# Optimization experiments

Measured on AMD Instinct MI355X. Metric: run time of the kernel, lower is better.

The kernel has to match this reference:

```python
import jax, jax.numpy as jnp
import numpy as np

B, N, C, DFF, NH, KNN = 4, 2048, 256, 1024, 4, 16


def _gelu(x):
    return jax.nn.gelu(x, approximate=False)  # torch nn.GELU default = exact erf


def _ln(x, g, b, eps=1e-5):
    m = jnp.mean(x, axis=-1, keepdims=True)
    v = jnp.mean((x - m) ** 2, axis=-1, keepdims=True)
    return (x - m) * jax.lax.rsqrt(v + eps) * g + b


def setup_inputs() -> dict:
    key = jax.random.key(0)
    ks = jax.random.split(key, 16)
    w = lambda k, shp: jax.random.normal(k, shp, jnp.float32) * 0.02
    return {
        "src1": jax.random.normal(ks[0], (B, C, N), jnp.float32),
        "src2": jax.random.normal(ks[1], (B, C, N), jnp.float32),
        "pos": jax.random.uniform(ks[2], (B, 3, N), jnp.float32),
        # input_proj Conv1d(C, C, 1)
        "Wp": w(ks[3], (C, C)), "bp": jnp.zeros((C,), jnp.float32),
        # rel_pos_encoder: Conv2d(3, C//4, 1) -> GELU -> Conv2d(C//4, 1, 1)
        "Wr1": w(ks[4], (C // 4, 3)), "br1": jnp.zeros((C // 4,), jnp.float32),
        "Wr2": w(ks[5], (1, C // 4)), "br2": jnp.zeros((1,), jnp.float32),
        # MultiheadAttention packed in-proj + out-proj
        "Wqkv": w(ks[6], (3 * C, C)), "bqkv": jnp.zeros((3 * C,), jnp.float32),
        "Wo": w(ks[7], (C, C)), "bo": jnp.zeros((C,), jnp.float32),
        # norms
        "g13": jnp.ones((C,), jnp.float32), "b13": jnp.zeros((C,), jnp.float32),
        "g12": jnp.ones((C,), jnp.float32), "b12": jnp.zeros((C,), jnp.float32),
        # FFN
        "W1": w(ks[8], (DFF, C)), "b1": jnp.zeros((DFF,), jnp.float32),
        "W2": w(ks[9], (C, DFF)), "b2": jnp.zeros((C,), jnp.float32),
    }


def reference(src1, src2, pos, Wp, bp, Wr1, br1, Wr2, br2, Wqkv, bqkv,
              Wo, bo, g13, b13, g12, b12, W1, b1, W2, b2):
    b, _, n = src1.shape
    c = Wp.shape[0]
    h = NH
    dh = c // h

    # input_proj (1x1 conv == matmul over channel dim); go to (b, n, c)
    s1 = jnp.einsum('oc,bcn->bno', Wp, src1) + bp
    s2 = jnp.einsum('oc,bcn->bno', Wp, src2) + bp

    # --- KNN + rel-pos bias ---
    p = pos.transpose(0, 2, 1)  # (b, n, 3)
    sq = jnp.sum(p * p, axis=-1)  # (b, n)
    dist = sq[:, :, None] + sq[:, None, :] - 2.0 * jnp.einsum('bnd,bmd->bnm', p, p)
    _, idx = jax.lax.top_k(-dist, KNN)  # (b, n, KNN) nearest (incl. self)
    knn_pos = jax.vmap(lambda pp, ii: pp[ii])(p, idx)  # (b, n, KNN, 3)
    rel = p[:, :, None, :] - knn_pos  # (b, n, KNN, 3)
    hid = _gelu(jnp.einsum('bnkd,od->bnko', rel, Wr1) + br1)
    bias_vals = (jnp.einsum('bnko,uo->bnku', hid, Wr2) + br2)[..., 0]  # (b, n, KNN)

    attn_bias = jnp.full((b, n, n), -jnp.inf, dtype=s1.dtype)
    bi = jnp.arange(b)[:, None, None]
    ri = jnp.arange(n)[None, :, None]
    attn_bias = attn_bias.at[bi, ri, idx].set(bias_vals)  # scatter along dim 2

    # --- pre-norm (norm13 shared for q and kv) ---
    x1 = _ln(s1, g13, b13)
    x2 = _ln(s2, g13, b13)

    # --- multihead attention with additive float mask ---
    Wq, Wk, Wv = jnp.split(Wqkv, 3, axis=0)
    bq, bk, bv = jnp.split(bqkv, 3)
    q = (x1 @ Wq.T + bq).reshape(b, n, h, dh)
    k = (x2 @ Wk.T + bk).reshape(b, n, h, dh)
    v = (x2 @ Wv.T + bv).reshape(b, n, h, dh)
    scores = jnp.einsum('bqhd,bkhd->bhqk', q, k) / jnp.sqrt(jnp.asarray(dh, s1.dtype))
    scores = scores + attn_bias[:, None, :, :]  # repeat_interleave(nhead) == head broadcast
    attn = jax.nn.softmax(scores, axis=-1)
    o = jnp.einsum('bhqk,bkhd->bqhd', attn, v).reshape(b, n, c) @ Wo.T + bo

    x1 = _ln(x1 + o, g12, b12)
    ff = _gelu(x1 @ W1.T + b1) @ W2.T + b2
    out = x1 + ff
    return out.transpose(0, 2, 1)  # (b, c, n)
```

## Files before the change

kernel.cpp:

```cpp
#include <hip/hip_runtime.h>
#include <hip/hip_bf16.h>
#include <math.h>

constexpr int kB = 4;
constexpr int kN = 2048;
constexpr int kC = 256;
constexpr int kDFF = 1024;
constexpr int kKNN = 16;
constexpr int kDH = 64;

typedef __attribute__((ext_vector_type(8))) short short8;
typedef __attribute__((ext_vector_type(4))) float float4v;

__device__ __forceinline__ float gelu_erf(float x) {
    return 0.5f * x * (1.0f + erff(x * 0.70710678118654752440f));
}

__device__ __forceinline__ short f2b(float f) {
    unsigned u = __float_as_uint(f);
    u = u + 0x7FFFu + ((u >> 16) & 1u);
    return (short)(u >> 16);
}

__device__ __forceinline__ float b2f(short h) {
    unsigned u = ((unsigned)(unsigned short)h) << 16;
    return __uint_as_float(u);
}

__global__ __launch_bounds__(256) void cvt_all(
    const float* __restrict__ Wqkv, const float* __restrict__ Wo,
    const float* __restrict__ W1, const float* __restrict__ W2,
    const float* __restrict__ Wp, short* __restrict__ dst)
{
    const int i = (blockIdx.x * 256 + threadIdx.x) * 8;
    if (i < 786432) {
        const float* src; int off;
        if (i < 196608)      { src = Wqkv; off = i; }
        else if (i < 262144) { src = Wo;   off = i - 196608; }
        else if (i < 524288) { src = W1;   off = i - 262144; }
        else                 { src = W2;   off = i - 524288; }
        short8 v;
        #pragma unroll
        for (int j = 0; j < 8; j++) v[j] = f2b(src[off + j]);
        *(short8*)&dst[i] = v;
    } else {
        const int off = i - 786432;
        short8 h, l;
        #pragma unroll
        for (int j = 0; j < 8; j++) {
            float v = Wp[off + j];
            short hh = f2b(v);
            h[j] = hh;
            l[j] = f2b(v - b2f(hh));
        }
        *(short8*)&dst[786432 + off] = h;
        *(short8*)&dst[851968 + off] = l;
    }
}

__global__ __launch_bounds__(256) void transpose_cvt(
    const float* __restrict__ src1, const float* __restrict__ src2,
    short* __restrict__ hiT, short* __restrict__ loT)
{
    __shared__ float tile[32][33];
    const int z = blockIdx.z;
    const float* in = (z < 4 ? src1 : src2) + (size_t)(z & 3) * kC * kN;
    const int n0 = blockIdx.x * 32;
    const int c0 = blockIdx.y * 32;
    const int tx = threadIdx.x;
    const int ty = threadIdx.y;
    #pragma unroll
    for (int i = 0; i < 32; i += 8)
        tile[ty + i][tx] = in[(size_t)(c0 + ty + i) * kN + (n0 + tx)];
    __syncthreads();
    #pragma unroll
    for (int i = 0; i < 32; i += 8) {
        float v = tile[tx][ty + i];
        short h = f2b(v);
        short l = f2b(v - b2f(h));
        size_t o = ((size_t)z * kN + (n0 + ty + i)) * kC + (c0 + tx);
        hiT[o] = h;
        loT[o] = l;
    }
}

__global__ __launch_bounds__(256) void proj_mfma(
    const short* __restrict__ Ahi, const short* __restrict__ Alo,
    const short* __restrict__ Whi, const short* __restrict__ Wlo,
    const float* __restrict__ bias, float* __restrict__ out)
{
    __shared__ __align__(16) short AsmH[64][40], AsmL[64][40];
    __shared__ __align__(16) short BsmH[64][40], BsmL[64][40];

    const int tid = threadIdx.x;
    const int n0 = blockIdx.x * 64;
    const size_t m0 = (size_t)blockIdx.y * 64;
    const int lane = tid & 63, wv = tid >> 6;
    const int lm = lane & 15, quad = lane >> 4;
    const int r = tid >> 2, q = tid & 3;

    float4v acc[4] = {};

    for (int k0 = 0; k0 < kC; k0 += 32) {
        *(short8*)&AsmH[r][q * 8] = *(const short8*)&Ahi[(m0 + r) * kC + k0 + q * 8];
        *(short8*)&AsmL[r][q * 8] = *(const short8*)&Alo[(m0 + r) * kC + k0 + q * 8];
        *(short8*)&BsmH[r][q * 8] = *(const short8*)&Whi[(size_t)(n0 + r) * kC + k0 + q * 8];
        *(short8*)&BsmL[r][q * 8] = *(const short8*)&Wlo[(size_t)(n0 + r) * kC + k0 + q * 8];
        __syncthreads();

        short8 ah = *(const short8*)&AsmH[wv * 16 + lm][quad * 8];
        short8 al = *(const short8*)&AsmL[wv * 16 + lm][quad * 8];
        #pragma unroll
        for (int j4 = 0; j4 < 4; j4++) {
            short8 bh = *(const short8*)&BsmH[j4 * 16 + lm][quad * 8];
            short8 bl = *(const short8*)&BsmL[j4 * 16 + lm][quad * 8];
            acc[j4] = __builtin_amdgcn_mfma_f32_16x16x32_bf16(al, bh, acc[j4], 0, 0, 0);
            acc[j4] = __builtin_amdgcn_mfma_f32_16x16x32_bf16(ah, bl, acc[j4], 0, 0, 0);
            acc[j4] = __builtin_amdgcn_mfma_f32_16x16x32_bf16(ah, bh, acc[j4], 0, 0, 0);
        }
        __syncthreads();
    }

    #pragma unroll
    for (int j4 = 0; j4 < 4; j4++) {
        const int n = n0 + j4 * 16 + lm;
        const float bn = bias[n];
        #pragma unroll
        for (int rg = 0; rg < 4; rg++) {
            const size_t m = m0 + wv * 16 + quad * 4 + rg;
            out[m * kC + n] = acc[j4][rg] + bn;
        }
    }
}

__global__ __launch_bounds__(256) void mfma_gemm_bf(
    const short* __restrict__ A, const short* __restrict__ W,
    const float* __restrict__ bias, const float* __restrict__ resid,
    float* __restrict__ out, short* __restrict__ outbf,
    int M, int Nout, int K, int epi)
{
    __shared__ __align__(16) short Asm[64][40];
    __shared__ __align__(16) short Bsm[64][40];

    const int tid = threadIdx.x;
    const int n0 = blockIdx.x * 64;
    const int m0 = blockIdx.y * 64;
    const int lane = tid & 63, wv = tid >> 6;
    const int lm = lane & 15, quad = lane >> 4;
    const int r = tid >> 2, q = tid & 3;

    float4v acc[4] = {};

    for (int k0 = 0; k0 < K; k0 += 32) {
        *(short8*)&Asm[r][q * 8] = *(const short8*)&A[(size_t)(m0 + r) * K + k0 + q * 8];
        *(short8*)&Bsm[r][q * 8] = *(const short8*)&W[(size_t)(n0 + r) * K + k0 + q * 8];
        __syncthreads();

        short8 af = *(const short8*)&Asm[wv * 16 + lm][quad * 8];
        #pragma unroll
        for (int j4 = 0; j4 < 4; j4++) {
            short8 bf = *(const short8*)&Bsm[j4 * 16 + lm][quad * 8];
            acc[j4] = __builtin_amdgcn_mfma_f32_16x16x32_bf16(af, bf, acc[j4], 0, 0, 0);
        }
        __syncthreads();
    }

    #pragma unroll
    for (int j4 = 0; j4 < 4; j4++) {
        const int n = n0 + j4 * 16 + lm;
        const float bn = bias[n];
        #pragma unroll
        for (int rg = 0; rg < 4; rg++) {
            const int m = m0 + wv * 16 + quad * 4 + rg;
            float v = acc[j4][rg] + bn;
            if (resid) v += resid[(size_t)m * Nout + n];
            if (epi == 1) v = gelu_erf(v);
            if (out)   out[(size_t)m * Nout + n] = v;
            if (outbf) outbf[(size_t)m * Nout + n] = f2b(v);
        }
    }
}

__global__ __launch_bounds__(256) void qkv_gemm(
    const short* __restrict__ x1bf, const short* __restrict__ x2bf,
    const short* __restrict__ Wqkvbf, const float* __restrict__ bqkv,
    float* __restrict__ qb, float* __restrict__ kvb)
{
    __shared__ __align__(16) short Asm[64][40];
    __shared__ __align__(16) short Bsm[64][40];

    const int n0g = blockIdx.x * 64;
    const int m0 = blockIdx.y * 64;
    const short* A; float* out; int Nout; int ncol0;
    if (n0g < 256) { A = x1bf; out = qb;  Nout = 256; ncol0 = n0g; }
    else           { A = x2bf; out = kvb; Nout = 512; ncol0 = n0g - 256; }

    const int tid = threadIdx.x;
    const int lane = tid & 63, wv = tid >> 6;
    const int lm = lane & 15, quad = lane >> 4;
    const int r = tid >> 2, q = tid & 3;

    float4v acc[4] = {};

    for (int k0 = 0; k0 < kC; k0 += 32) {
        *(short8*)&Asm[r][q * 8] = *(const short8*)&A[(size_t)(m0 + r) * kC + k0 + q * 8];
        *(short8*)&Bsm[r][q * 8] = *(const short8*)&Wqkvbf[(size_t)(n0g + r) * kC + k0 + q * 8];
        __syncthreads();

        short8 af = *(const short8*)&Asm[wv * 16 + lm][quad * 8];
        #pragma unroll
        for (int j4 = 0; j4 < 4; j4++) {
            short8 bf = *(const short8*)&Bsm[j4 * 16 + lm][quad * 8];
            acc[j4] = __builtin_amdgcn_mfma_f32_16x16x32_bf16(af, bf, acc[j4], 0, 0, 0);
        }
        __syncthreads();
    }

    #pragma unroll
    for (int j4 = 0; j4 < 4; j4++) {
        const int nc = ncol0 + j4 * 16 + lm;
        const float bn = bqkv[n0g + j4 * 16 + lm];
        #pragma unroll
        for (int rg = 0; rg < 4; rg++) {
            const int m = m0 + wv * 16 + quad * 4 + rg;
            out[(size_t)m * Nout + nc] = acc[j4][rg] + bn;
        }
    }
}

__global__ __launch_bounds__(256) void ln_kernel(
    float* __restrict__ x, short* __restrict__ xbf,
    const float* __restrict__ g, const float* __restrict__ bb)
{
    const size_t row = blockIdx.x;
    const int t = threadIdx.x;
    float v = x[row * kC + t];

    __shared__ float red4[4];
    float s = v;
    #pragma unroll
    for (int off = 32; off; off >>= 1) s += __shfl_xor(s, off, 64);
    if ((t & 63) == 0) red4[t >> 6] = s;
    __syncthreads();
    float mean = (red4[0] + red4[1] + red4[2] + red4[3]) * (1.0f / kC);

    float d = v - mean;
    float s2 = d * d;
    #pragma unroll
    for (int off = 32; off; off >>= 1) s2 += __shfl_xor(s2, off, 64);
    __syncthreads();
    if ((t & 63) == 0) red4[t >> 6] = s2;
    __syncthreads();
    float var = (red4[0] + red4[1] + red4[2] + red4[3]) * (1.0f / kC);

    float r = 1.0f / sqrtf(var + 1e-5f);
    float o = d * r * g[t] + bb[t];
    x[row * kC + t] = o;
    xbf[row * kC + t] = f2b(o);
}

#define KNN_RESCAN(CH, BM, BI)                                        \
    do {                                                              \
        float nb_ = 1e30f; int ni_ = kN;                              \
        _Pragma("unroll")                                             \
        for (int c8_ = 0; c8_ < 8; c8_++) {                           \
            int c_ = (CH) * 8 + c8_;                                  \
            float dd_ = (mask & (1u << c_)) ? 1e30f : cd[c_];         \
            if (dd_ < nb_) { nb_ = dd_; ni_ = c_ * 64 + lane; }       \
        }                                                             \
        BM = nb_; BI = ni_;                                           \
    } while (0)

__global__ __launch_bounds__(512) void knn_kernel(
    const float* __restrict__ pos,
    const float* __restrict__ Wr1, const float* __restrict__ br1,
    const float* __restrict__ Wr2, const float* __restrict__ br2,
    int* __restrict__ idx_out, float* __restrict__ bias_out)
{
    __shared__ float px[kN], py[kN], pz[kN];
    __shared__ int selS[8][kKNN];

    const int b = blockIdx.y;
    const int t = threadIdx.x;
    const int lane = t & 63, wv = t >> 6;
    const int n = blockIdx.x * 8 + wv;

    const float* pb = pos + (size_t)b * 3 * kN;
    for (int m = t; m < kN; m += 512) {
        px[m] = pb[m]; py[m] = pb[kN + m]; pz[m] = pb[2 * kN + m];
    }
    __syncthreads();

    const float qx = px[n], qy = py[n], qz = pz[n];
    const float qsq = __fadd_rn(__fadd_rn(__fmul_rn(qx, qx), __fmul_rn(qy, qy)),
                                __fmul_rn(qz, qz));

    float cd[32];
    float bm0 = 1e30f, bm1 = 1e30f, bm2 = 1e30f, bm3 = 1e30f;
    int bi0 = kN, bi1 = kN, bi2 = kN, bi3 = kN;
    #pragma unroll
    for (int c8 = 0; c8 < 8; c8++) {
        {
            const int c = c8, m = c * 64 + lane;
            float ax = px[m], ay = py[m], az = pz[m];
            float asq = __fadd_rn(__fadd_rn(__fmul_rn(ax, ax), __fmul_rn(ay, ay)), __fmul_rn(az, az));
            float dot = __fadd_rn(__fadd_rn(__fmul_rn(qx, ax), __fmul_rn(qy, ay)), __fmul_rn(qz, az));
            float d = __fsub_rn(__fadd_rn(qsq, asq), __fmul_rn(2.0f, dot));
            cd[c] = d;
            if (d < bm0) { bm0 = d; bi0 = m; }
        }
        {
            const int c = c8 + 8, m = c * 64 + lane;
            float ax = px[m], ay = py[m], az = pz[m];
            float asq = __fadd_rn(__fadd_rn(__fmul_rn(ax, ax), __fmul_rn(ay, ay)), __fmul_rn(az, az));
            float dot = __fadd_rn(__fadd_rn(__fmul_rn(qx, ax), __fmul_rn(qy, ay)), __fmul_rn(qz, az));
            float d = __fsub_rn(__fadd_rn(qsq, asq), __fmul_rn(2.0f, dot));
            cd[c] = d;
            if (d < bm1) { bm1 = d; bi1 = m; }
        }
        {
            const int c = c8 + 16, m = c * 64 + lane;
            float ax = px[m], ay = py[m], az = pz[m];
            float asq = __fadd_rn(__fadd_rn(__fmul_rn(ax, ax), __fmul_rn(ay, ay)), __fmul_rn(az, az));
            float dot = __fadd_rn(__fadd_rn(__fmul_rn(qx, ax), __fmul_rn(qy, ay)), __fmul_rn(qz, az));
            float d = __fsub_rn(__fadd_rn(qsq, asq), __fmul_rn(2.0f, dot));
            cd[c] = d;
            if (d < bm2) { bm2 = d; bi2 = m; }
        }
        {
            const int c = c8 + 24, m = c * 64 + lane;
            float ax = px[m], ay = py[m], az = pz[m];
            float asq = __fadd_rn(__fadd_rn(__fmul_rn(ax, ax), __fmul_rn(ay, ay)), __fmul_rn(az, az));
            float dot = __fadd_rn(__fadd_rn(__fmul_rn(qx, ax), __fmul_rn(qy, ay)), __fmul_rn(qz, az));
            float d = __fsub_rn(__fadd_rn(qsq, asq), __fmul_rn(2.0f, dot));
            cd[c] = d;
            if (d < bm3) { bm3 = d; bi3 = m; }
        }
    }

    unsigned mask = 0;
    for (int r = 0; r < kKNN; r++) {
        float best = bm0; int bid = bi0;
        if (bm1 < best) { best = bm1; bid = bi1; }
        if (bm2 < best) { best = bm2; bid = bi2; }
        if (bm3 < best) { best = bm3; bid = bi3; }

        #pragma unroll
        for (int off = 1; off < 64; off <<= 1) {
            float od = __shfl_xor(best, off, 64);
            int   oi = __shfl_xor(bid, off, 64);
            if (od < best || (od == best && oi < bid)) { best = od; bid = oi; }
        }
        if (lane == 0) selS[wv][r] = bid;
        if ((bid & 63) == lane) mask |= 1u << (bid >> 6);

        if (r < kKNN - 1) {
            const int sch = __builtin_amdgcn_readfirstlane(bid >> 9);
            switch (sch) {
                case 0:  KNN_RESCAN(0, bm0, bi0); break;
                case 1:  KNN_RESCAN(1, bm1, bi1); break;
                case 2:  KNN_RESCAN(2, bm2, bi2); break;
                default: KNN_RESCAN(3, bm3, bi3); break;
            }
        }
    }

    const int k = lane >> 2;
    const int part = lane & 3;
    const int m = selS[wv][k];
    const float rx = qx - px[m], ry = qy - py[m], rz = qz - pz[m];
    float partial = 0.0f;
    #pragma unroll
    for (int jj = 0; jj < 16; jj++) {
        int o = part * 16 + jj;
        float h = rx * Wr1[o * 3 + 0] + ry * Wr1[o * 3 + 1] +
                  rz * Wr1[o * 3 + 2] + br1[o];
        partial += gelu_erf(h) * Wr2[o];
    }
    partial += __shfl_xor(partial, 1, 64);
    partial += __shfl_xor(partial, 2, 64);
    if (part == 0) {
        size_t o = ((size_t)b * kN + n) * kKNN + k;
        idx_out[o] = m;
        bias_out[o] = partial + br2[0];
    }
}

__global__ __launch_bounds__(256) void attn_kernel(
    const float* __restrict__ q, const float* __restrict__ kv,
    const int* __restrict__ idx, const float* __restrict__ bias,
    short* __restrict__ obf)
{
    const int n = blockIdx.x;
    const int b = blockIdx.y;
    const int t = threadIdx.x;
    const int h = t >> 6;
    const int d = t & 63;

    const size_t row = (size_t)b * kN + n;
    const float qv = q[row * kC + h * kDH + d];

    __shared__ int   sidx[kKNN];
    __shared__ float sb[kKNN];
    if (t < kKNN) { sidx[t] = idx[row * kKNN + t]; sb[t] = bias[row * kKNN + t]; }
    __syncthreads();

    float sc[kKNN];
    #pragma unroll
    for (int j = 0; j < kKNN; j++) {
        size_t kr = (size_t)b * kN + sidx[j];
        float p = qv * kv[kr * 512 + h * kDH + d];
        #pragma unroll
        for (int off = 32; off; off >>= 1) p += __shfl_xor(p, off, 64);
        sc[j] = p * 0.125f + sb[j];
    }
    float mx = sc[0];
    #pragma unroll
    for (int j = 1; j < kKNN; j++) mx = fmaxf(mx, sc[j]);
    float den = 0.0f;
    #pragma unroll
    for (int j = 0; j < kKNN; j++) { sc[j] = expf(sc[j] - mx); den += sc[j]; }
    const float inv = 1.0f / den;
    float o = 0.0f;
    #pragma unroll
    for (int j = 0; j < kKNN; j++) {
        size_t kr = (size_t)b * kN + sidx[j];
        o += sc[j] * inv * kv[kr * 512 + kC + h * kDH + d];
    }
    obf[row * kC + h * kDH + d] = f2b(o);
}

__global__ __launch_bounds__(256) void transpose_f32(
    const float* __restrict__ z, float* __restrict__ out)
{
    __shared__ float tile[32][33];
    const int b = blockIdx.z;
    const int n0 = blockIdx.x * 32;
    const int c0 = blockIdx.y * 32;
    const int tx = threadIdx.x;
    const int ty = threadIdx.y;
    #pragma unroll
    for (int i = 0; i < 32; i += 8)
        tile[ty + i][tx] = z[(size_t)b * kN * kC + (size_t)(n0 + ty + i) * kC + (c0 + tx)];
    __syncthreads();
    #pragma unroll
    for (int i = 0; i < 32; i += 8)
        out[(size_t)b * kC * kN + (size_t)(c0 + ty + i) * kN + (n0 + tx)] =
            tile[tx][ty + i];
}

extern "C" void kernel_launch(void* const* d_in, const int* in_sizes, int n_in,
                              void* d_out, int out_size, void* d_ws, size_t ws_size,
                              hipStream_t stream)
{
    const float* src1 = (const float*)d_in[0];
    const float* src2 = (const float*)d_in[1];
    const float* pos  = (const float*)d_in[2];
    const float* Wp   = (const float*)d_in[3];
    const float* bp   = (const float*)d_in[4];
    const float* Wr1  = (const float*)d_in[5];
    const float* br1  = (const float*)d_in[6];
    const float* Wr2  = (const float*)d_in[7];
    const float* br2  = (const float*)d_in[8];
    const float* Wqkv = (const float*)d_in[9];
    const float* bqkv = (const float*)d_in[10];
    const float* Wo   = (const float*)d_in[11];
    const float* bo   = (const float*)d_in[12];
    const float* g13  = (const float*)d_in[13];
    const float* b13  = (const float*)d_in[14];
    const float* g12  = (const float*)d_in[15];
    const float* b12  = (const float*)d_in[16];
    const float* W1   = (const float*)d_in[17];
    const float* b1   = (const float*)d_in[18];
    const float* W2   = (const float*)d_in[19];
    const float* b2   = (const float*)d_in[20];
    float* out = (float*)d_out;

    const size_t S = (size_t)kB * kN * kC;
    float* ws = (float*)d_ws;
    float* x1  = ws;
    float* s2  = ws + S;
    float* qb  = ws + 2 * S;
    float* kvb = ws + 3 * S;
    float* yb  = ws + 2 * S;
    float* zb  = ws + S;
    short* srcThi = (short*)(ws + 2 * S);
    short* srcTlo = (short*)(ws + 3 * S);
    short* x1bf = (short*)(ws + 5 * S);
    short* x2bf = (short*)(ws + 5 * S) + S;
    short* ybf  = (short*)(ws + 6 * S);
    short* obf  = (short*)(ws + 6 * S) + S;
    short* hbf  = (short*)(ws + 3 * S);
    int*   idxb  = (int*)(ws + 7 * S);
    float* biasb = ws + 7 * S + (size_t)kB * kN * kKNN;
    short* wbf    = (short*)(ws + 7 * S + 2 * (size_t)kB * kN * kKNN);
    short* Wqkvbf = wbf;
    short* Wobf   = wbf + 196608;
    short* W1bf   = wbf + 262144;
    short* W2bf   = wbf + 524288;
    short* Wphi   = wbf + 786432;
    short* Wplo   = wbf + 851968;

    const int M = kB * kN;

    cvt_all<<<416, 256, 0, stream>>>(Wqkv, Wo, W1, W2, Wp, wbf);

    transpose_cvt<<<dim3(kN / 32, kC / 32, 8), dim3(32, 8), 0, stream>>>(
        src1, src2, srcThi, srcTlo);
    proj_mfma<<<dim3(kC / 64, 2 * M / 64), 256, 0, stream>>>(
        srcThi, srcTlo, Wphi, Wplo, bp, x1);

    ln_kernel<<<2 * M, 256, 0, stream>>>(x1, x1bf, g13, b13);

    knn_kernel<<<dim3(kN / 8, kB), 512, 0, stream>>>(pos, Wr1, br1, Wr2, br2, idxb, biasb);

    qkv_gemm<<<dim3(12, M / 64), 256, 0, stream>>>(x1bf, x2bf, Wqkvbf, bqkv, qb, kvb);

    attn_kernel<<<dim3(kN, kB), 256, 0, stream>>>(qb, kvb, idxb, biasb, obf);

    mfma_gemm_bf<<<dim3(kC / 64, M / 64), 256, 0, stream>>>(
        obf, Wobf, bo, x1, yb, nullptr, M, kC, kC, 0);
    ln_kernel<<<M, 256, 0, stream>>>(yb, ybf, g12, b12);

    mfma_gemm_bf<<<dim3(kDFF / 64, M / 64), 256, 0, stream>>>(
        ybf, W1bf, b1, nullptr, nullptr, hbf, M, kDFF, kC, 1);
    mfma_gemm_bf<<<dim3(kC / 64, M / 64), 256, 0, stream>>>(
        hbf, W2bf, b2, yb, zb, nullptr, M, kC, kDFF, 0);

    transpose_f32<<<dim3(kN / 32, kC / 32, kB), dim3(32, 8), 0, stream>>>(zb, out);
}
```

Measured before the change: 302.2 us.

## Fuse output transpose into FFN2 GEMM and deepen GEMM K-tiles to 64

The second FFN GEMM now transposes its tile through shared memory and writes the (b, c, n) output directly, which removes the separate transpose kernel and the round trip through an intermediate buffer. The generic and QKV GEMMs also stage 64-wide K slices instead of 32, with two MFMAs per sync, halving the number of barrier iterations. The cost is more shared memory per block, plus the extra transpose tile in the fused kernel, which may reduce occupancy.

```diff
diff --git a/kernel.cpp b/kernel.cpp
--- a/kernel.cpp
+++ b/kernel.cpp
@@ -139,8 +139,8 @@
     float* __restrict__ out, short* __restrict__ outbf,
     int M, int Nout, int K, int epi)
 {
-    __shared__ __align__(16) short Asm[64][40];
-    __shared__ __align__(16) short Bsm[64][40];
+    __shared__ __align__(16) short Asm[64][72];
+    __shared__ __align__(16) short Bsm[64][72];
 
     const int tid = threadIdx.x;
     const int n0 = blockIdx.x * 64;
@@ -151,16 +151,23 @@
 
     float4v acc[4] = {};
 
-    for (int k0 = 0; k0 < K; k0 += 32) {
-        *(short8*)&Asm[r][q * 8] = *(const short8*)&A[(size_t)(m0 + r) * K + k0 + q * 8];
-        *(short8*)&Bsm[r][q * 8] = *(const short8*)&W[(size_t)(n0 + r) * K + k0 + q * 8];
-        __syncthreads();
-
-        short8 af = *(const short8*)&Asm[wv * 16 + lm][quad * 8];
+    for (int k0 = 0; k0 < K; k0 += 64) {
+        const short* ap = &A[(size_t)(m0 + r) * K + k0 + q * 16];
+        *(short8*)&Asm[r][q * 16]     = *(const short8*)ap;
+        *(short8*)&Asm[r][q * 16 + 8] = *(const short8*)(ap + 8);
+        const short* wp = &W[(size_t)(n0 + r) * K + k0 + q * 16];
+        *(short8*)&Bsm[r][q * 16]     = *(const short8*)wp;
+        *(short8*)&Bsm[r][q * 16 + 8] = *(const short8*)(wp + 8);
+        __syncthreads();
+
+        short8 af0 = *(const short8*)&Asm[wv * 16 + lm][quad * 8];
+        short8 af1 = *(const short8*)&Asm[wv * 16 + lm][32 + quad * 8];
         #pragma unroll
         for (int j4 = 0; j4 < 4; j4++) {
-            short8 bf = *(const short8*)&Bsm[j4 * 16 + lm][quad * 8];
-            acc[j4] = __builtin_amdgcn_mfma_f32_16x16x32_bf16(af, bf, acc[j4], 0, 0, 0);
+            short8 bf0 = *(const short8*)&Bsm[j4 * 16 + lm][quad * 8];
+            short8 bf1 = *(const short8*)&Bsm[j4 * 16 + lm][32 + quad * 8];
+            acc[j4] = __builtin_amdgcn_mfma_f32_16x16x32_bf16(af0, bf0, acc[j4], 0, 0, 0);
+            acc[j4] = __builtin_amdgcn_mfma_f32_16x16x32_bf16(af1, bf1, acc[j4], 0, 0, 0);
         }
         __syncthreads();
     }
@@ -186,8 +193,8 @@
     const short* __restrict__ Wqkvbf, const float* __restrict__ bqkv,
     float* __restrict__ qb, float* __restrict__ kvb)
 {
-    __shared__ __align__(16) short Asm[64][40];
-    __shared__ __align__(16) short Bsm[64][40];
+    __shared__ __align__(16) short Asm[64][72];
+    __shared__ __align__(16) short Bsm[64][72];
 
     const int n0g = blockIdx.x * 64;
     const int m0 = blockIdx.y * 64;
@@ -202,16 +209,23 @@
 
     float4v acc[4] = {};
 
-    for (int k0 = 0; k0 < kC; k0 += 32) {
-        *(short8*)&Asm[r][q * 8] = *(const short8*)&A[(size_t)(m0 + r) * kC + k0 + q * 8];
-        *(short8*)&Bsm[r][q * 8] = *(const short8*)&Wqkvbf[(size_t)(n0g + r) * kC + k0 + q * 8];
-        __syncthreads();
-
-        short8 af = *(const short8*)&Asm[wv * 16 + lm][quad * 8];
+    for (int k0 = 0; k0 < kC; k0 += 64) {
+        const short* ap = &A[(size_t)(m0 + r) * kC + k0 + q * 16];
+        *(short8*)&Asm[r][q * 16]     = *(const short8*)ap;
+        *(short8*)&Asm[r][q * 16 + 8] = *(const short8*)(ap + 8);
+        const short* wp = &Wqkvbf[(size_t)(n0g + r) * kC + k0 + q * 16];
+        *(short8*)&Bsm[r][q * 16]     = *(const short8*)wp;
+        *(short8*)&Bsm[r][q * 16 + 8] = *(const short8*)(wp + 8);
+        __syncthreads();
+
+        short8 af0 = *(const short8*)&Asm[wv * 16 + lm][quad * 8];
+        short8 af1 = *(const short8*)&Asm[wv * 16 + lm][32 + quad * 8];
         #pragma unroll
         for (int j4 = 0; j4 < 4; j4++) {
-            short8 bf = *(const short8*)&Bsm[j4 * 16 + lm][quad * 8];
-            acc[j4] = __builtin_amdgcn_mfma_f32_16x16x32_bf16(af, bf, acc[j4], 0, 0, 0);
+            short8 bf0 = *(const short8*)&Bsm[j4 * 16 + lm][quad * 8];
+            short8 bf1 = *(const short8*)&Bsm[j4 * 16 + lm][32 + quad * 8];
+            acc[j4] = __builtin_amdgcn_mfma_f32_16x16x32_bf16(af0, bf0, acc[j4], 0, 0, 0);
+            acc[j4] = __builtin_amdgcn_mfma_f32_16x16x32_bf16(af1, bf1, acc[j4], 0, 0, 0);
         }
         __syncthreads();
     }
@@ -225,6 +239,76 @@
             const int m = m0 + wv * 16 + quad * 4 + rg;
             out[(size_t)m * Nout + nc] = acc[j4][rg] + bn;
         }
+    }
+}
+
+__global__ __launch_bounds__(256) void ffn2_gemm_tr(
+    const short* __restrict__ A, const short* __restrict__ W,
+    const float* __restrict__ bias, const float* __restrict__ resid,
+    float* __restrict__ out)
+{
+    __shared__ __align__(16) short Asm[64][72];
+    __shared__ __align__(16) short Bsm[64][72];
+    __shared__ float T[64][65];
+
+    constexpr int K = kDFF;
+    constexpr int Nout = kC;
+    const int tid = threadIdx.x;
+    const int n0 = blockIdx.x * 64;
+    const int m0 = blockIdx.y * 64;
+    const int lane = tid & 63, wv = tid >> 6;
+    const int lm = lane & 15, quad = lane >> 4;
+    const int r = tid >> 2, q = tid & 3;
+
+    float4v acc[4] = {};
+
+    for (int k0 = 0; k0 < K; k0 += 64) {
+        const short* ap = &A[(size_t)(m0 + r) * K + k0 + q * 16];
+        *(short8*)&Asm[r][q * 16]     = *(const short8*)ap;
+        *(short8*)&Asm[r][q * 16 + 8] = *(const short8*)(ap + 8);
+        const short* wp = &W[(size_t)(n0 + r) * K + k0 + q * 16];
+        *(short8*)&Bsm[r][q * 16]     = *(const short8*)wp;
+        *(short8*)&Bsm[r][q * 16 + 8] = *(const short8*)(wp + 8);
+        __syncthreads();
+
+        short8 af0 = *(const short8*)&Asm[wv * 16 + lm][quad * 8];
+        short8 af1 = *(const short8*)&Asm[wv * 16 + lm][32 + quad * 8];
+        #pragma unroll
+        for (int j4 = 0; j4 < 4; j4++) {
+            short8 bf0 = *(const short8*)&Bsm[j4 * 16 + lm][quad * 8];
+            short8 bf1 = *(const short8*)&Bsm[j4 * 16 + lm][32 + quad * 8];
+            acc[j4] = __builtin_amdgcn_mfma_f32_16x16x32_bf16(af0, bf0, acc[j4], 0, 0, 0);
+            acc[j4] = __builtin_amdgcn_mfma_f32_16x16x32_bf16(af1, bf1, acc[j4], 0, 0, 0);
+        }
+        __syncthreads();
+    }
+
+    #pragma unroll
+    for (int j4 = 0; j4 < 4; j4++) {
+        const int nloc = j4 * 16 + lm;
+        const float bn = bias[n0 + nloc];
+        #pragma unroll
+        for (int rg = 0; rg < 4; rg++) {
+            const int mloc = wv * 16 + quad * 4 + rg;
+            float v = acc[j4][rg] + bn;
+            v += resid[(size_t)(m0 + mloc) * Nout + (n0 + nloc)];
+            T[nloc][mloc] = v;
+        }
+    }
+    __syncthreads();
+
+    const int bidx = m0 >> 11;
+    const int nb = m0 & 2047;
+    const int nloc = tid >> 2;
+    const int l4 = tid & 3;
+    float* orow = out + (size_t)bidx * kC * kN + (size_t)(n0 + nloc) * kN + nb;
+    #pragma unroll
+    for (int i = 0; i < 4; i++) {
+        const int mloc = l4 * 4 + i * 16;
+        float4v v4;
+        v4[0] = T[nloc][mloc];     v4[1] = T[nloc][mloc + 1];
+        v4[2] = T[nloc][mloc + 2]; v4[3] = T[nloc][mloc + 3];
+        *(float4v*)&orow[mloc] = v4;
     }
 }
 
@@ -428,25 +512,6 @@
         o += sc[j] * inv * kv[kr * 512 + kC + h * kDH + d];
     }
     obf[row * kC + h * kDH + d] = f2b(o);
-}
-
-__global__ __launch_bounds__(256) void transpose_f32(
-    const float* __restrict__ z, float* __restrict__ out)
-{
-    __shared__ float tile[32][33];
-    const int b = blockIdx.z;
-    const int n0 = blockIdx.x * 32;
-    const int c0 = blockIdx.y * 32;
-    const int tx = threadIdx.x;
-    const int ty = threadIdx.y;
-    #pragma unroll
-    for (int i = 0; i < 32; i += 8)
-        tile[ty + i][tx] = z[(size_t)b * kN * kC + (size_t)(n0 + ty + i) * kC + (c0 + tx)];
-    __syncthreads();
-    #pragma unroll
-    for (int i = 0; i < 32; i += 8)
-        out[(size_t)b * kC * kN + (size_t)(c0 + ty + i) * kN + (n0 + tx)] =
-            tile[tx][ty + i];
 }
 
 extern "C" void kernel_launch(void* const* d_in, const int* in_sizes, int n_in,
@@ -483,7 +548,6 @@
     float* qb  = ws + 2 * S;
     float* kvb = ws + 3 * S;
     float* yb  = ws + 2 * S;
-    float* zb  = ws + S;
     short* srcThi = (short*)(ws + 2 * S);
     short* srcTlo = (short*)(ws + 3 * S);
     short* x1bf = (short*)(ws + 5 * S);
@@ -524,8 +588,6 @@
 
     mfma_gemm_bf<<<dim3(kDFF / 64, M / 64), 256, 0, stream>>>(
         ybf, W1bf, b1, nullptr, nullptr, hbf, M, kDFF, kC, 1);
-    mfma_gemm_bf<<<dim3(kC / 64, M / 64), 256, 0, stream>>>(
-        hbf, W2bf, b2, yb, zb, nullptr, M, kC, kDFF, 0);
-
-    transpose_f32<<<dim3(kN / 32, kC / 32, kB), dim3(32, 8), 0, stream>>>(zb, out);
-}
+    ffn2_gemm_tr<<<dim3(kC / 64, M / 64), 256, 0, stream>>>(
+        hbf, W2bf, b2, yb, out);
+}
```

Result: faster. 291.3 us (-3.6%).
